# Kernel tuning notes

Measured on AMD Instinct MI355X. Metric: run time of the kernel, lower is better.

The kernel has to match this reference:

```python
import jax, jax.numpy as jnp
import numpy as np

B, C, H, W = 8, 192, 128, 128
HEADS = 16
EPS = 1e-12  # F.normalize eps


def setup_inputs() -> dict:
    key = jax.random.key(0)
    k1, k2, k3, k4 = jax.random.split(key, 4)
    s = 0.02
    return {
        "x": jax.random.normal(k1, (B, C, H, W), dtype=jnp.float32),
        "w_qkv": jax.random.normal(k2, (3 * C, C), dtype=jnp.float32) * s,
        "w_dw": jax.random.normal(k3, (C, 1, 3, 3), dtype=jnp.float32) * s,
        "w_proj": jax.random.normal(k4, (C, C), dtype=jnp.float32) * s,
        "temperature": jnp.ones((HEADS, 1, 1), dtype=jnp.float32),
    }


def reference(x, w_qkv, w_dw, w_proj, temperature):
    b, c, h, w = x.shape
    heads = HEADS
    hd = c // heads  # per-head channel dim
    hw = h * w

    # 1x1 conv qkv projection: [b, 3c, h, w]
    qkv = jnp.einsum('bchw,oc->bohw', x, w_qkv)
    q, k, v = jnp.split(qkv, 3, axis=1)

    def to_heads(t):
        return t.reshape(b, heads, hd, hw)  # b head c (h w)

    q, k, v = to_heads(q), to_heads(k), to_heads(v)

    # L2-normalize along spatial dim (matches F.normalize with eps clamp)
    q = q / jnp.maximum(jnp.linalg.norm(q, axis=-1, keepdims=True), EPS)
    k = k / jnp.maximum(jnp.linalg.norm(k, axis=-1, keepdims=True), EPS)

    # channel-wise attention: [b, head, hd, hd]
    attn = jnp.einsum('bhcn,bhdn->bhcd', q, k) * temperature
    attn = jax.nn.softmax(attn, axis=-1)

    out = jnp.einsum('bhcd,bhdn->bhcn', attn, v)  # [b, head, hd, hw]
    out = out.reshape(b, c, h, w)

    # depthwise 3x3 conv, padding=1
    out = jax.lax.conv_general_dilated(
        out, w_dw, window_strides=(1, 1), padding=((1, 1), (1, 1)),
        dimension_numbers=('NCHW', 'OIHW', 'NCHW'), feature_group_count=c)

    # 1x1 conv projection
    out = jnp.einsum('bchw,oc->bohw', out, w_proj)
    return out
```

## Files before the change

kernel.cpp:

```cpp
#include <hip/hip_runtime.h>

#define B_   8
#define C_   192
#define HW_  16384
#define W_   128
#define NH_  16
#define HD_  12

#define OFF_G      0u
#define OFF_WQKV   1179648u
#define OFF_WDW    1622016u
#define OFF_TEMP   1628928u
#define OFF_WPROJ  1629184u
#define OFF_M      1702912u
#define OFF_Y      2292736u

typedef __attribute__((ext_vector_type(8))) __bf16 bf16x8;
typedef __attribute__((ext_vector_type(8))) short  short8;
typedef __attribute__((ext_vector_type(4))) short  short4v;
typedef __attribute__((ext_vector_type(4))) float  floatx4;

__device__ __forceinline__ unsigned short f2bfu(float f) {
  union { float f; unsigned u; } v; v.f = f;
  unsigned r = (v.u + 0x7FFFu + ((v.u >> 16) & 1u)) >> 16;
  return (unsigned short)r;
}
__device__ __forceinline__ float bfu2f(unsigned short h) {
  union { unsigned u; float f; } v; v.u = ((unsigned)h) << 16;
  return v.f;
}
__device__ __forceinline__ bool bfmode(const void* temp) {
  return ((const unsigned*)temp)[0] != 0x3F800000u;
}
__device__ __forceinline__ float in_ld(const void* p, int i, bool bf) {
  return bf ? bfu2f(((const unsigned short*)p)[i]) : ((const float*)p)[i];
}
__device__ __forceinline__ floatx4 mfma16(short8 a, short8 b, floatx4 c) {
  union U { short8 s; bf16x8 b; } ua, ub;
  ua.s = a; ub.s = b;
  return __builtin_amdgcn_mfma_f32_16x16x32_bf16(ua.b, ub.b, c, 0, 0, 0);
}
__device__ __forceinline__ short8 row_frag(const void* x, bool bf, long elemoff) {
  short8 r;
  if (bf) {
    r = *(const short8*)((const unsigned short*)x + elemoff);
  } else {
    const float4* p4 = (const float4*)((const float*)x + elemoff);
    float4 a = p4[0], b = p4[1];
    r[0] = (short)f2bfu(a.x); r[1] = (short)f2bfu(a.y);
    r[2] = (short)f2bfu(a.z); r[3] = (short)f2bfu(a.w);
    r[4] = (short)f2bfu(b.x); r[5] = (short)f2bfu(b.y);
    r[6] = (short)f2bfu(b.z); r[7] = (short)f2bfu(b.w);
  }
  return r;
}

__global__ __launch_bounds__(256) void k_init(const void* wqkv, const void* wdw,
                                              const void* wproj, const void* temp,
                                              unsigned char* ws) {
  bool bf = bfmode(temp);
  int idx = blockIdx.x * 256 + threadIdx.x;
  if (idx < 294912) { ((float*)(ws + OFF_G))[idx] = 0.f; return; }
  int i = idx - 294912;
  if (i < 110592) { ((float*)(ws + OFF_WQKV))[i] = in_ld(wqkv, i, bf); return; }
  i -= 110592;
  if (i < 1728) { ((float*)(ws + OFF_WDW))[i] = in_ld(wdw, i, bf); return; }
  i -= 1728;
  if (i < 16) { ((float*)(ws + OFF_TEMP))[i] = in_ld(temp, i, bf); return; }
  i -= 16;
  if (i < 36864) {
    unsigned short* wp = (unsigned short*)(ws + OFF_WPROJ);
    wp[i] = bf ? ((const unsigned short*)wproj)[i] : f2bfu(((const float*)wproj)[i]);
  }
}

__global__ __launch_bounds__(256) void k_gram(const void* x, const void* temp,
                                              unsigned char* ws) {
  bool bf = bfmode(temp);
  float* G = (float*)(ws + OFF_G);
  int b = blockIdx.x >> 5, grp = blockIdx.x & 31;
  int tid = threadIdx.x;
  int w = tid >> 6, lane = tid & 63, m = lane & 15, q = lane >> 4;
  long xb = (long)b * C_ * HW_;
  __shared__ __align__(16) short xs[C_][136];
  floatx4 acc[3][12];
  floatx4 zz = {0.f, 0.f, 0.f, 0.f};
  for (int i = 0; i < 3; ++i)
    for (int t = 0; t < 12; ++t) acc[i][t] = zz;
  for (int sl = 0; sl < 4; ++sl) {
    int px0 = (grp * 4 + sl) * 128;
    if (sl) __syncthreads();
    for (int i = 0; i < 12; ++i) {
      int chunk = i * 256 + tid;
      int c = chunk >> 4, p8 = chunk & 15;
      short8 v = row_frag(x, bf, xb + (long)c * HW_ + px0 + p8 * 8);
      *(short8*)&xs[c][p8 * 8] = v;
    }
    __syncthreads();
    for (int ks = 0; ks < 4; ++ks) {
      int col = ks * 32 + q * 8;
      short8 A0 = *(const short8*)&xs[(3 * w + 0) * 16 + m][col];
      short8 A1 = *(const short8*)&xs[(3 * w + 1) * 16 + m][col];
      short8 A2 = *(const short8*)&xs[(3 * w + 2) * 16 + m][col];
      for (int t = 0; t < 12; ++t) {
        short8 F = *(const short8*)&xs[t * 16 + m][col];
        acc[0][t] = mfma16(A0, F, acc[0][t]);
        acc[1][t] = mfma16(A1, F, acc[1][t]);
        acc[2][t] = mfma16(A2, F, acc[2][t]);
      }
    }
  }
  for (int i = 0; i < 3; ++i)
    for (int t = 0; t < 12; ++t)
      for (int r = 0; r < 4; ++r)
        atomicAdd(&G[((long)b * C_ + (3 * w + i) * 16 + q * 4 + r) * C_ + t * 16 + m],
                  acc[i][t][r]);
}

__global__ __launch_bounds__(256) void k_attn(unsigned char* ws) {
  int b = blockIdx.x >> 4, h = blockIdx.x & 15;
  int tid = threadIdx.x;
  const float* G  = (const float*)(ws + OFF_G) + (long)b * C_ * C_;
  const float* Wf = (const float*)(ws + OFF_WQKV);
  const float* Wq = Wf + (h * HD_) * C_;
  const float* Wk = Wf + (C_ + h * HD_) * C_;
  const float* Wv = Wf + (2 * C_ + h * HD_) * C_;
  float tmprt = ((const float*)(ws + OFF_TEMP))[h];
  unsigned short* Mh = (unsigned short*)(ws + OFF_M) + ((long)b * C_ + h * HD_) * C_;

  __shared__ float Gs[32][C_ + 1];
  __shared__ float tq[HD_][C_], tk[HD_][C_];
  __shared__ float Sm[HD_][HD_], Aw[HD_][HD_], nq[HD_], nk[HD_];

  for (int jblk = 0; jblk < 6; ++jblk) {
    for (int i = tid; i < 32 * C_; i += 256) {
      int jj = i / C_, a = i - jj * C_;
      Gs[jj][a] = G[(jblk * 32 + jj) * C_ + a];
    }
    __syncthreads();
    for (int i = tid; i < 2 * HD_ * 32; i += 256) {
      int jj = i & 31, rest = i >> 5;
      int c = rest % HD_, which = rest / HD_;
      const float* Wrow = (which ? Wk : Wq) + c * C_;
      float s = 0.f;
      for (int a = 0; a < C_; ++a) s += Wrow[a] * Gs[jj][a];
      float (*dst)[C_] = which ? tk : tq;
      dst[c][jblk * 32 + jj] = s;
    }
    __syncthreads();
  }
  if (tid < 144) {
    int c = tid / HD_, d = tid - c * HD_;
    float s = 0.f;
    for (int a = 0; a < C_; ++a) s += tq[c][a] * Wk[d * C_ + a];
    Sm[c][d] = s;
  } else if (tid < 156) {
    int c = tid - 144; float s = 0.f;
    for (int a = 0; a < C_; ++a) s += tq[c][a] * Wq[c * C_ + a];
    nq[c] = s;
  } else if (tid < 168) {
    int c = tid - 156; float s = 0.f;
    for (int a = 0; a < C_; ++a) s += tk[c][a] * Wk[c * C_ + a];
    nk[c] = s;
  }
  __syncthreads();
  if (tid < HD_) {
    int c = tid;
    float qn = fmaxf(sqrtf(fmaxf(nq[c], 0.f)), 1e-12f);
    float L[HD_], mx = -1e30f;
    for (int d = 0; d < HD_; ++d) {
      float kn = fmaxf(sqrtf(fmaxf(nk[d], 0.f)), 1e-12f);
      L[d] = Sm[c][d] / (qn * kn) * tmprt;
      mx = fmaxf(mx, L[d]);
    }
    float ssum = 0.f;
    for (int d = 0; d < HD_; ++d) { L[d] = __expf(L[d] - mx); ssum += L[d]; }
    float inv = 1.f / ssum;
    for (int d = 0; d < HD_; ++d) Aw[c][d] = L[d] * inv;
  }
  __syncthreads();
  for (int i = tid; i < HD_ * C_; i += 256) {
    int c = i / C_, j = i - c * C_;
    float s = 0.f;
    for (int d = 0; d < HD_; ++d) s += Aw[c][d] * Wv[d * C_ + j];
    Mh[c * C_ + j] = f2bfu(s);
  }
}

__global__ __launch_bounds__(256) void k_mx(const void* x, const void* temp,
                                            unsigned char* ws) {
  bool bf = bfmode(temp);
  const unsigned short* Mb = (const unsigned short*)(ws + OFF_M);
  unsigned short* y = (unsigned short*)(ws + OFF_Y);
  int b = blockIdx.x >> 7, px0 = (blockIdx.x & 127) * 128;
  int tid = threadIdx.x;
  int w = tid >> 6, lane = tid & 63, m = lane & 15, q = lane >> 4;
  long xb = (long)b * C_ * HW_;
  __shared__ __align__(16) short xsT[128][200];
  for (int i = 0; i < 3; ++i) {
    int chunk = i * 256 + tid;
    int p8 = chunk & 15, cq = chunk >> 4;
    short8 r0 = row_frag(x, bf, xb + (long)(cq * 4 + 0) * HW_ + px0 + p8 * 8);
    short8 r1 = row_frag(x, bf, xb + (long)(cq * 4 + 1) * HW_ + px0 + p8 * 8);
    short8 r2 = row_frag(x, bf, xb + (long)(cq * 4 + 2) * HW_ + px0 + p8 * 8);
    short8 r3 = row_frag(x, bf, xb + (long)(cq * 4 + 3) * HW_ + px0 + p8 * 8);
    for (int j = 0; j < 8; ++j) {
      short4v v = { r0[j], r1[j], r2[j], r3[j] };
      *(short4v*)&xsT[p8 * 8 + j][cq * 4] = v;
    }
  }
  __syncthreads();
  floatx4 acc[3][8];
  floatx4 zz = {0.f, 0.f, 0.f, 0.f};
  for (int i = 0; i < 3; ++i)
    for (int pt = 0; pt < 8; ++pt) acc[i][pt] = zz;
  for (int k = 0; k < 6; ++k) {
    int c0 = k * 32;
    const unsigned short* Mrow = Mb + (long)b * C_ * C_ + c0 + q * 8;
    short8 A0 = *(const short8*)(Mrow + ((3 * w + 0) * 16 + m) * C_);
    short8 A1 = *(const short8*)(Mrow + ((3 * w + 1) * 16 + m) * C_);
    short8 A2 = *(const short8*)(Mrow + ((3 * w + 2) * 16 + m) * C_);
    for (int pt = 0; pt < 8; ++pt) {
      short8 Bf = *(const short8*)&xsT[pt * 16 + m][c0 + q * 8];
      acc[0][pt] = mfma16(A0, Bf, acc[0][pt]);
      acc[1][pt] = mfma16(A1, Bf, acc[1][pt]);
      acc[2][pt] = mfma16(A2, Bf, acc[2][pt]);
    }
  }
  for (int i = 0; i < 3; ++i) {
    int rowb = (3 * w + i) * 16 + q * 4;
    for (int pt = 0; pt < 8; ++pt) {
      int px = px0 + pt * 16 + m;
      for (int rg = 0; rg < 4; ++rg)
        y[((long)b * C_ + rowb + rg) * HW_ + px] = f2bfu(acc[i][pt][rg]);
    }
  }
}

__global__ __launch_bounds__(256) void k_out(const void* temp, unsigned char* ws,
                                             void* out) {
  bool bf = bfmode(temp);
  const unsigned short* y = (const unsigned short*)(ws + OFF_Y);
  const float* wdw = (const float*)(ws + OFF_WDW);
  const unsigned short* Wp = (const unsigned short*)(ws + OFF_WPROJ);
  int b = blockIdx.x >> 7, irow = blockIdx.x & 127;
  int tid = threadIdx.x;
  __shared__ unsigned short dT[C_][130];
  {
    int oct = tid & 15, cq = tid >> 4;
    int p0 = oct * 8;
    for (int c = cq; c < C_; c += 16) {
      float wv[9];
      for (int t = 0; t < 9; ++t) wv[t] = wdw[c * 9 + t];
      float a0[8];
      for (int i = 0; i < 8; ++i) a0[i] = 0.f;
      const unsigned short* yc = y + ((long)b * C_ + c) * HW_;
      for (int dy = 0; dy < 3; ++dy) {
        int rr = irow + dy - 1;
        if (rr < 0 || rr > 127) continue;
        const unsigned short* yr = yc + rr * W_;
        float v[10];
        v[0] = (p0 == 0) ? 0.f : bfu2f(yr[p0 - 1]);
        union { uint4 u; unsigned short s[8]; } uu;
        uu.u = *(const uint4*)(yr + p0);
        for (int i = 0; i < 8; ++i) v[1 + i] = bfu2f(uu.s[i]);
        v[9] = (p0 + 8 >= W_) ? 0.f : bfu2f(yr[p0 + 8]);
        for (int dx = 0; dx < 3; ++dx) {
          float wc = wv[dy * 3 + dx];
          for (int i = 0; i < 8; ++i) a0[i] += wc * v[i + dx];
        }
      }
      for (int i = 0; i < 8; ++i) dT[c][p0 + i] = f2bfu(a0[i]);
    }
  }
  __syncthreads();
  int wave = tid >> 6, lane = tid & 63;
  int m = lane & 15, q = lane >> 4;
  floatx4 acc[12][2];
  floatx4 zz = {0.f, 0.f, 0.f, 0.f};
  for (int r = 0; r < 12; ++r) { acc[r][0] = zz; acc[r][1] = zz; }
  int pA = wave * 32 + m, pB = pA + 16;
  for (int k = 0; k < 6; ++k) {
    int c0 = k * 32 + q * 8;
    short8 B0, B1;
    for (int j = 0; j < 8; ++j) {
      B0[j] = (short)dT[c0 + j][pA];
      B1[j] = (short)dT[c0 + j][pB];
    }
    for (int r = 0; r < 12; ++r) {
      short8 A = *(const short8*)(Wp + (r * 16 + m) * C_ + c0);
      acc[r][0] = mfma16(A, B0, acc[r][0]);
      acc[r][1] = mfma16(A, B1, acc[r][1]);
    }
  }
  long ob = (long)b * C_ * HW_ + irow * W_;
  for (int r = 0; r < 12; ++r) {
    int o = r * 16 + q * 4;
    for (int rg = 0; rg < 4; ++rg) {
      long off = ob + (long)(o + rg) * HW_;
      float v0 = acc[r][0][rg], v1 = acc[r][1][rg];
      if (bf) {
        ((unsigned short*)out)[off + pA] = f2bfu(v0);
        ((unsigned short*)out)[off + pB] = f2bfu(v1);
      } else {
        ((float*)out)[off + pA] = v0;
        ((float*)out)[off + pB] = v1;
      }
    }
  }
}

extern "C" void kernel_launch(void* const* d_in, const int* in_sizes, int n_in,
                              void* d_out, int out_size, void* d_ws, size_t ws_size,
                              hipStream_t stream) {
  const void* x     = d_in[0];
  const void* wqkv  = d_in[1];
  const void* wdw   = d_in[2];
  const void* wproj = d_in[3];
  const void* temp  = d_in[4];
  unsigned char* ws = (unsigned char*)d_ws;
  k_init<<<dim3(1735), dim3(256), 0, stream>>>(wqkv, wdw, wproj, temp, ws);
  k_gram<<<dim3(256), dim3(256), 0, stream>>>(x, temp, ws);
  k_attn<<<dim3(128), dim3(256), 0, stream>>>(ws);
  k_mx<<<dim3(1024), dim3(256), 0, stream>>>(x, temp, ws);
  k_out<<<dim3(1024), dim3(256), 0, stream>>>(temp, ws, d_out);
}
```

Baseline: 401.0 us.

## Store intermediate channel-last and fuse depthwise conv into projection fragments

k_mx now transposes its output tile through shared memory and writes the intermediate in pixel-major, channel-contiguous layout. k_out computes the depthwise 3x3 conv directly into the MFMA B fragments from that layout, using transposed bf16 depthwise weights staged in LDS, instead of building a separate LDS tile first. The final output is also staged through LDS so stores are vectorized and coalesced rather than scattered scalar writes. This trades extra LDS passes and syncs, and a rounding of the fp32 output through bf16 in fp32 mode, for fewer uncoalesced global accesses.

```diff
diff --git a/kernel.cpp b/kernel.cpp
--- a/kernel.cpp
+++ b/kernel.cpp
@@ -9,11 +9,11 @@
 
 #define OFF_G      0u
 #define OFF_WQKV   1179648u
-#define OFF_WDW    1622016u
-#define OFF_TEMP   1628928u
-#define OFF_WPROJ  1629184u
-#define OFF_M      1702912u
-#define OFF_Y      2292736u
+#define OFF_WDWT   1622016u
+#define OFF_TEMP   1625600u
+#define OFF_WPROJ  1625856u
+#define OFF_M      1699584u
+#define OFF_Y      2289408u
 
 typedef __attribute__((ext_vector_type(8))) __bf16 bf16x8;
 typedef __attribute__((ext_vector_type(8))) short  short8;
@@ -64,7 +64,11 @@
   int i = idx - 294912;
   if (i < 110592) { ((float*)(ws + OFF_WQKV))[i] = in_ld(wqkv, i, bf); return; }
   i -= 110592;
-  if (i < 1728) { ((float*)(ws + OFF_WDW))[i] = in_ld(wdw, i, bf); return; }
+  if (i < 1728) {
+    int t = i / 192, c = i - t * 192;
+    ((unsigned short*)(ws + OFF_WDWT))[i] = f2bfu(in_ld(wdw, c * 9 + t, bf));
+    return;
+  }
   i -= 1728;
   if (i < 16) { ((float*)(ws + OFF_TEMP))[i] = in_ld(temp, i, bf); return; }
   i -= 16;
@@ -191,12 +195,12 @@
                                             unsigned char* ws) {
   bool bf = bfmode(temp);
   const unsigned short* Mb = (const unsigned short*)(ws + OFF_M);
-  unsigned short* y = (unsigned short*)(ws + OFF_Y);
+  unsigned short* yTg = (unsigned short*)(ws + OFF_Y);
   int b = blockIdx.x >> 7, px0 = (blockIdx.x & 127) * 128;
   int tid = threadIdx.x;
   int w = tid >> 6, lane = tid & 63, m = lane & 15, q = lane >> 4;
   long xb = (long)b * C_ * HW_;
-  __shared__ __align__(16) short xsT[128][200];
+  __shared__ __align__(16) short smem[25728];
   for (int i = 0; i < 3; ++i) {
     int chunk = i * 256 + tid;
     int p8 = chunk & 15, cq = chunk >> 4;
@@ -206,7 +210,7 @@
     short8 r3 = row_frag(x, bf, xb + (long)(cq * 4 + 3) * HW_ + px0 + p8 * 8);
     for (int j = 0; j < 8; ++j) {
       short4v v = { r0[j], r1[j], r2[j], r3[j] };
-      *(short4v*)&xsT[p8 * 8 + j][cq * 4] = v;
+      *(short4v*)&smem[(p8 * 8 + j) * 200 + cq * 4] = v;
     }
   }
   __syncthreads();
@@ -221,71 +225,78 @@
     short8 A1 = *(const short8*)(Mrow + ((3 * w + 1) * 16 + m) * C_);
     short8 A2 = *(const short8*)(Mrow + ((3 * w + 2) * 16 + m) * C_);
     for (int pt = 0; pt < 8; ++pt) {
-      short8 Bf = *(const short8*)&xsT[pt * 16 + m][c0 + q * 8];
+      short8 Bf = *(const short8*)&smem[(pt * 16 + m) * 200 + c0 + q * 8];
       acc[0][pt] = mfma16(A0, Bf, acc[0][pt]);
       acc[1][pt] = mfma16(A1, Bf, acc[1][pt]);
       acc[2][pt] = mfma16(A2, Bf, acc[2][pt]);
     }
   }
+  __syncthreads();
   for (int i = 0; i < 3; ++i) {
     int rowb = (3 * w + i) * 16 + q * 4;
     for (int pt = 0; pt < 8; ++pt) {
-      int px = px0 + pt * 16 + m;
+      int px = pt * 16 + m;
       for (int rg = 0; rg < 4; ++rg)
-        y[((long)b * C_ + rowb + rg) * HW_ + px] = f2bfu(acc[i][pt][rg]);
-    }
+        smem[(rowb + rg) * 134 + px] = (short)f2bfu(acc[i][pt][rg]);
+    }
+  }
+  __syncthreads();
+  long pbase = (long)b * HW_ + px0;
+  for (int j = 0; j < 12; ++j) {
+    int chunk = j * 256 + tid;
+    int px = chunk / 24, c8 = chunk - px * 24;
+    short8 v;
+    for (int jj = 0; jj < 8; ++jj) v[jj] = smem[(c8 * 8 + jj) * 134 + px];
+    *(short8*)(yTg + (pbase + px) * C_ + c8 * 8) = v;
   }
 }
 
 __global__ __launch_bounds__(256) void k_out(const void* temp, unsigned char* ws,
                                              void* out) {
   bool bf = bfmode(temp);
-  const unsigned short* y = (const unsigned short*)(ws + OFF_Y);
-  const float* wdw = (const float*)(ws + OFF_WDW);
+  const unsigned short* yT = (const unsigned short*)(ws + OFF_Y);
+  const unsigned short* wT = (const unsigned short*)(ws + OFF_WDWT);
   const unsigned short* Wp = (const unsigned short*)(ws + OFF_WPROJ);
   int b = blockIdx.x >> 7, irow = blockIdx.x & 127;
   int tid = threadIdx.x;
-  __shared__ unsigned short dT[C_][130];
-  {
-    int oct = tid & 15, cq = tid >> 4;
-    int p0 = oct * 8;
-    for (int c = cq; c < C_; c += 16) {
-      float wv[9];
-      for (int t = 0; t < 9; ++t) wv[t] = wdw[c * 9 + t];
-      float a0[8];
-      for (int i = 0; i < 8; ++i) a0[i] = 0.f;
-      const unsigned short* yc = y + ((long)b * C_ + c) * HW_;
-      for (int dy = 0; dy < 3; ++dy) {
-        int rr = irow + dy - 1;
-        if (rr < 0 || rr > 127) continue;
-        const unsigned short* yr = yc + rr * W_;
-        float v[10];
-        v[0] = (p0 == 0) ? 0.f : bfu2f(yr[p0 - 1]);
-        union { uint4 u; unsigned short s[8]; } uu;
-        uu.u = *(const uint4*)(yr + p0);
-        for (int i = 0; i < 8; ++i) v[1 + i] = bfu2f(uu.s[i]);
-        v[9] = (p0 + 8 >= W_) ? 0.f : bfu2f(yr[p0 + 8]);
-        for (int dx = 0; dx < 3; ++dx) {
-          float wc = wv[dy * 3 + dx];
-          for (int i = 0; i < 8; ++i) a0[i] += wc * v[i + dx];
-        }
-      }
-      for (int i = 0; i < 8; ++i) dT[c][p0 + i] = f2bfu(a0[i]);
-    }
-  }
-  __syncthreads();
-  int wave = tid >> 6, lane = tid & 63;
-  int m = lane & 15, q = lane >> 4;
+  __shared__ __align__(16) short smem[1728 + 96 * 136];
+  short* wTs = smem;
+  short* os  = smem + 1728;
+  for (int i = tid; i < 1728; i += 256) wTs[i] = (short)wT[i];
+  __syncthreads();
+  int w = tid >> 6, lane = tid & 63, m = lane & 15, q = lane >> 4;
+  int pA = w * 32 + m, pB = pA + 16;
   floatx4 acc[12][2];
   floatx4 zz = {0.f, 0.f, 0.f, 0.f};
   for (int r = 0; r < 12; ++r) { acc[r][0] = zz; acc[r][1] = zz; }
-  int pA = wave * 32 + m, pB = pA + 16;
+  long ybase = (long)b * HW_;
   for (int k = 0; k < 6; ++k) {
     int c0 = k * 32 + q * 8;
+    float d0[8], d1[8];
+    for (int j = 0; j < 8; ++j) { d0[j] = 0.f; d1[j] = 0.f; }
+    for (int dy = 0; dy < 3; ++dy) {
+      int rr = irow + dy - 1;
+      if (rr < 0 || rr > 127) continue;
+      const unsigned short* yr = yT + (ybase + rr * W_) * C_;
+      for (int dx = 0; dx < 3; ++dx) {
+        short8 wv = *(const short8*)&wTs[(dy * 3 + dx) * C_ + c0];
+        float wf[8];
+        for (int j = 0; j < 8; ++j) wf[j] = bfu2f((unsigned short)wv[j]);
+        int pa = pA + dx - 1, pb = pB + dx - 1;
+        if (pa >= 0) {
+          short8 yv = *(const short8*)(yr + pa * C_ + c0);
+          for (int j = 0; j < 8; ++j) d0[j] += wf[j] * bfu2f((unsigned short)yv[j]);
+        }
+        if (pb < W_) {
+          short8 yv = *(const short8*)(yr + pb * C_ + c0);
+          for (int j = 0; j < 8; ++j) d1[j] += wf[j] * bfu2f((unsigned short)yv[j]);
+        }
+      }
+    }
     short8 B0, B1;
     for (int j = 0; j < 8; ++j) {
-      B0[j] = (short)dT[c0 + j][pA];
-      B1[j] = (short)dT[c0 + j][pB];
+      B0[j] = (short)f2bfu(d0[j]);
+      B1[j] = (short)f2bfu(d1[j]);
     }
     for (int r = 0; r < 12; ++r) {
       short8 A = *(const short8*)(Wp + (r * 16 + m) * C_ + c0);
@@ -294,17 +305,31 @@
     }
   }
   long ob = (long)b * C_ * HW_ + irow * W_;
-  for (int r = 0; r < 12; ++r) {
-    int o = r * 16 + q * 4;
-    for (int rg = 0; rg < 4; ++rg) {
-      long off = ob + (long)(o + rg) * HW_;
-      float v0 = acc[r][0][rg], v1 = acc[r][1][rg];
+  for (int h = 0; h < 2; ++h) {
+    __syncthreads();
+    for (int r = h * 6; r < h * 6 + 6; ++r) {
+      int o = r * 16 + q * 4 - h * 96;
+      for (int rg = 0; rg < 4; ++rg) {
+        os[(o + rg) * 136 + pA] = (short)f2bfu(acc[r][0][rg]);
+        os[(o + rg) * 136 + pB] = (short)f2bfu(acc[r][1][rg]);
+      }
+    }
+    __syncthreads();
+    for (int j = 0; j < 6; ++j) {
+      int chunk = j * 256 + tid;
+      int cl = chunk >> 4, p8 = chunk & 15;
+      short8 v = *(const short8*)&os[cl * 136 + p8 * 8];
+      long off = ob + (long)(h * 96 + cl) * HW_ + p8 * 8;
       if (bf) {
-        ((unsigned short*)out)[off + pA] = f2bfu(v0);
-        ((unsigned short*)out)[off + pB] = f2bfu(v1);
+        *(short8*)((unsigned short*)out + off) = v;
       } else {
-        ((float*)out)[off + pA] = v0;
-        ((float*)out)[off + pB] = v1;
+        float* op = (float*)out + off;
+        float4 f0 = { bfu2f((unsigned short)v[0]), bfu2f((unsigned short)v[1]),
+                      bfu2f((unsigned short)v[2]), bfu2f((unsigned short)v[3]) };
+        float4 f1 = { bfu2f((unsigned short)v[4]), bfu2f((unsigned short)v[5]),
+                      bfu2f((unsigned short)v[6]), bfu2f((unsigned short)v[7]) };
+        *(float4*)op = f0;
+        *(float4*)(op + 4) = f1;
       }
     }
   }
```

New measurement: 417.3 us. 4.1% more time.
